# Kernel optimization log

Hardware: AMD Instinct MI355X
Metric: run time of the kernel (lower is better)

Reference implementation:

```python
import jax, jax.numpy as jnp
import numpy as np


def setup_inputs() -> dict:
    key = jax.random.key(0)
    k1, k2, k3 = jax.random.split(key, 3)
    B, N, D = 64, 2048, 1024
    output = jax.random.normal(k1, (B, 1, D), dtype=jnp.float32)
    context = jax.random.normal(k2, (B, N, D), dtype=jnp.float32)
    # nn.Linear(2*dim, dim): weight [dim, 2*dim], bias [dim]
    W_out = jax.random.normal(k3, (D, 2 * D), dtype=jnp.float32) * (1.0 / np.sqrt(2 * D))
    b_out = jnp.zeros((D,), dtype=jnp.float32)
    return {"output": output, "context": context, "W_out": W_out, "b_out": b_out}


def reference(output, context, W_out, b_out):
    B, q, D = output.shape  # q == 1
    N = context.shape[1]
    # scores: (B, q, N) = output @ context^T
    attn = jnp.einsum('bqd,bnd->bqn', output, context)
    attn = jax.nn.softmax(attn, axis=-1)
    # mix: (B, q, D)
    mix = jnp.einsum('bqn,bnd->bqd', attn, context)
    combined = jnp.concatenate([mix, output], axis=-1)  # (B, q, 2D)
    out = jnp.tanh(jnp.einsum('bqe,de->bqd', combined, W_out) + b_out)
    return (out, attn)
```

## Files before the change

### kernel.cpp

```cpp
#include <hip/hip_runtime.h>
#include <cmath>

#define BATCH 64
#define NCTX 2048
#define DIM 1024
#define CHUNKS 16
#define ROWS_PER_CHUNK (NCTX / CHUNKS)
#define ROWS_PER_WAVE (ROWS_PER_CHUNK / 4)

typedef float f4_t __attribute__((ext_vector_type(4)));

__global__ __launch_bounds__(256) void attn_phase1(
    const float* __restrict__ q,
    const float* __restrict__ ctx,
    float* __restrict__ scores,
    float* __restrict__ part_m,
    float* __restrict__ part_l,
    float* __restrict__ part_o)
{
    const int blk  = blockIdx.x;
    const int b    = blk / CHUNKS;
    const int c    = blk % CHUNKS;
    const int tid  = threadIdx.x;
    const int wave = tid >> 6;
    const int lane = tid & 63;

    f4_t qf[4];
    const float* qb = q + (size_t)b * DIM;
    #pragma unroll
    for (int j = 0; j < 4; ++j)
        qf[j] = *reinterpret_cast<const f4_t*>(qb + lane * 4 + 256 * j);

    float m = -INFINITY, l = 0.f;
    f4_t o[4];
    #pragma unroll
    for (int j = 0; j < 4; ++j) o[j] = (f4_t)(0.f);

    const int row0 = c * ROWS_PER_CHUNK + wave * ROWS_PER_WAVE;
    const float* cb = ctx + (size_t)b * NCTX * DIM;
    float* sc = scores + (size_t)b * NCTX;

    for (int i = 0; i < ROWS_PER_WAVE; i += 4) {
        f4_t cf[4][4];
        #pragma unroll
        for (int r = 0; r < 4; ++r) {
            const float* cr = cb + (size_t)(row0 + i + r) * DIM + lane * 4;
            #pragma unroll
            for (int j = 0; j < 4; ++j)
                cf[r][j] = __builtin_nontemporal_load(
                    reinterpret_cast<const f4_t*>(cr + 256 * j));
        }

        float s[4];
        #pragma unroll
        for (int r = 0; r < 4; ++r) {
            float d0 = qf[0].x * cf[r][0].x + qf[0].y * cf[r][0].y
                     + qf[0].z * cf[r][0].z + qf[0].w * cf[r][0].w;
            float d1 = qf[1].x * cf[r][1].x + qf[1].y * cf[r][1].y
                     + qf[1].z * cf[r][1].z + qf[1].w * cf[r][1].w;
            float d2 = qf[2].x * cf[r][2].x + qf[2].y * cf[r][2].y
                     + qf[2].z * cf[r][2].z + qf[2].w * cf[r][2].w;
            float d3 = qf[3].x * cf[r][3].x + qf[3].y * cf[r][3].y
                     + qf[3].z * cf[r][3].z + qf[3].w * cf[r][3].w;
            s[r] = (d0 + d1) + (d2 + d3);
        }

        #pragma unroll
        for (int off = 32; off >= 1; off >>= 1) {
            s[0] += __shfl_xor(s[0], off, 64);
            s[1] += __shfl_xor(s[1], off, 64);
            s[2] += __shfl_xor(s[2], off, 64);
            s[3] += __shfl_xor(s[3], off, 64);
        }

        {
            float sv = (lane == 1) ? s[1] : (lane == 2) ? s[2]
                     : (lane == 3) ? s[3] : s[0];
            if (lane < 4) sc[row0 + i + lane] = sv;
        }

        const float mx = fmaxf(fmaxf(s[0], s[1]), fmaxf(s[2], s[3]));
        const float m_new = fmaxf(m, mx);
        if (m_new > m) {
            const float a = __expf(m - m_new);
            l *= a;
            #pragma unroll
            for (int j = 0; j < 4; ++j) o[j] *= a;
            m = m_new;
        }
        const float p0 = __expf(s[0] - m);
        const float p1 = __expf(s[1] - m);
        const float p2 = __expf(s[2] - m);
        const float p3 = __expf(s[3] - m);
        l += (p0 + p1) + (p2 + p3);
        #pragma unroll
        for (int j = 0; j < 4; ++j) {
            o[j].x += p0 * cf[0][j].x + p1 * cf[1][j].x
                    + p2 * cf[2][j].x + p3 * cf[3][j].x;
            o[j].y += p0 * cf[0][j].y + p1 * cf[1][j].y
                    + p2 * cf[2][j].y + p3 * cf[3][j].y;
            o[j].z += p0 * cf[0][j].z + p1 * cf[1][j].z
                    + p2 * cf[2][j].z + p3 * cf[3][j].z;
            o[j].w += p0 * cf[0][j].w + p1 * cf[1][j].w
                    + p2 * cf[2][j].w + p3 * cf[3][j].w;
        }
    }

    __shared__ float wm[4], wl[4];
    __shared__ float o_lds[4 * DIM];
    if (lane == 0) { wm[wave] = m; wl[wave] = l; }
    __syncthreads();

    const float Mb = fmaxf(fmaxf(wm[0], wm[1]), fmaxf(wm[2], wm[3]));
    float Lb = 0.f;
    #pragma unroll
    for (int w = 0; w < 4; ++w) Lb += wl[w] * __expf(wm[w] - Mb);

    const float aw = __expf(m - Mb);
    #pragma unroll
    for (int j = 0; j < 4; ++j) {
        f4_t t = o[j] * aw;
        *reinterpret_cast<f4_t*>(&o_lds[wave * DIM + lane * 4 + 256 * j]) = t;
    }
    __syncthreads();

    {
        const int e = tid * 4;
        f4_t s0 = *reinterpret_cast<const f4_t*>(&o_lds[0 * DIM + e]);
        f4_t s1 = *reinterpret_cast<const f4_t*>(&o_lds[1 * DIM + e]);
        f4_t s2 = *reinterpret_cast<const f4_t*>(&o_lds[2 * DIM + e]);
        f4_t s3 = *reinterpret_cast<const f4_t*>(&o_lds[3 * DIM + e]);
        f4_t r = (s0 + s1) + (s2 + s3);
        *reinterpret_cast<f4_t*>(&part_o[((size_t)b * CHUNKS + c) * DIM + e]) = r;
    }
    if (tid == 0) {
        part_m[b * CHUNKS + c] = Mb;
        part_l[b * CHUNKS + c] = Lb;
    }
}

__global__ __launch_bounds__(256) void attn_phase2(
    const float* __restrict__ scores,
    const float* __restrict__ part_m,
    const float* __restrict__ part_l,
    const float* __restrict__ part_o,
    float* __restrict__ mix,
    float* __restrict__ attn_out)
{
    const int b    = blockIdx.x >> 2;
    const int part = blockIdx.x & 3;
    const int tid  = threadIdx.x;

    float M = -INFINITY;
    #pragma unroll
    for (int i = 0; i < CHUNKS; ++i) M = fmaxf(M, part_m[b * CHUNKS + i]);

    float w[CHUNKS];
    float L = 0.f;
    #pragma unroll
    for (int i = 0; i < CHUNKS; ++i) {
        w[i] = __expf(part_m[b * CHUNKS + i] - M);
        L += part_l[b * CHUNKS + i] * w[i];
    }
    const float invL = 1.f / L;

    {
        const int e = part * 256 + tid;
        float acc = 0.f;
        #pragma unroll
        for (int i = 0; i < CHUNKS; ++i)
            acc += part_o[((size_t)b * CHUNKS + i) * DIM + e] * w[i];
        mix[(size_t)b * DIM + e] = acc * invL;
    }

    #pragma unroll
    for (int t = 0; t < 2; ++t) {
        const int n = part * 512 + t * 256 + tid;
        attn_out[(size_t)b * NCTX + n] =
            __expf(scores[(size_t)b * NCTX + n] - M) * invL;
    }
}

#define BT 4
#define DT 32
__global__ __launch_bounds__(256) void attn_phase3(
    const float* __restrict__ mix,
    const float* __restrict__ q,
    const float* __restrict__ W,
    const float* __restrict__ bias,
    float* __restrict__ out)
{
    const int d_chunk = blockIdx.x % (DIM / DT);
    const int b_chunk = blockIdx.x / (DIM / DT);
    const int d0 = d_chunk * DT;
    const int b0 = b_chunk * BT;
    const int tid  = threadIdx.x;
    const int wave = tid >> 6;
    const int lane = tid & 63;

    __shared__ float comb[BT * 2 * DIM];
    for (int i = tid; i < BT * 2 * DIM; i += 256) {
        const int bl = i >> 11;
        const int e  = i & 2047;
        comb[i] = (e < DIM) ? mix[(size_t)(b0 + bl) * DIM + e]
                            : q[(size_t)(b0 + bl) * DIM + (e - DIM)];
    }
    __syncthreads();

    const int d_base = d0 + wave * (DT / 4);
    #pragma unroll
    for (int g = 0; g < 2; ++g) {
        const int dg = d_base + g * 4;
        float acc[4][BT];
        #pragma unroll
        for (int di = 0; di < 4; ++di)
            #pragma unroll
            for (int bl = 0; bl < BT; ++bl) acc[di][bl] = 0.f;

        for (int kk = 0; kk < 2 * DIM; kk += 256) {
            f4_t wv[4];
            #pragma unroll
            for (int di = 0; di < 4; ++di)
                wv[di] = *reinterpret_cast<const f4_t*>(
                    W + (size_t)(dg + di) * (2 * DIM) + kk + lane * 4);
            #pragma unroll
            for (int bl = 0; bl < BT; ++bl) {
                f4_t cv = *reinterpret_cast<const f4_t*>(
                    &comb[bl * 2 * DIM + kk + lane * 4]);
                #pragma unroll
                for (int di = 0; di < 4; ++di) {
                    acc[di][bl] += wv[di].x * cv.x;
                    acc[di][bl] += wv[di].y * cv.y;
                    acc[di][bl] += wv[di].z * cv.z;
                    acc[di][bl] += wv[di].w * cv.w;
                }
            }
        }

        float myval = 0.f;
        #pragma unroll
        for (int di = 0; di < 4; ++di) {
            #pragma unroll
            for (int bl = 0; bl < BT; ++bl) {
                float v = acc[di][bl];
                #pragma unroll
                for (int off = 32; off >= 1; off >>= 1)
                    v += __shfl_xor(v, off, 64);
                if (lane == di * BT + bl) myval = v;
            }
        }
        if (lane < 16) {
            const int di = lane >> 2;
            const int bl = lane & 3;
            const int d  = dg + di;
            out[(size_t)(b0 + bl) * DIM + d] = tanhf(myval + bias[d]);
        }
    }
}

extern "C" void kernel_launch(void* const* d_in, const int* in_sizes, int n_in,
                              void* d_out, int out_size, void* d_ws, size_t ws_size,
                              hipStream_t stream) {
    const float* q    = (const float*)d_in[0];
    const float* ctx  = (const float*)d_in[1];
    const float* W    = (const float*)d_in[2];
    const float* bias = (const float*)d_in[3];

    float* out_main = (float*)d_out;
    float* attn_out = (float*)d_out + (size_t)BATCH * DIM;

    float* ws      = (float*)d_ws;
    float* scores  = ws;
    float* part_m  = scores + (size_t)BATCH * NCTX;
    float* part_l  = part_m + BATCH * CHUNKS;
    float* part_o  = part_l + BATCH * CHUNKS;
    float* mix     = part_o + (size_t)BATCH * CHUNKS * DIM;

    attn_phase1<<<BATCH * CHUNKS, 256, 0, stream>>>(q, ctx, scores,
                                                    part_m, part_l, part_o);
    attn_phase2<<<BATCH * 4, 256, 0, stream>>>(scores, part_m, part_l, part_o,
                                               mix, attn_out);
    attn_phase3<<<(DIM / DT) * (BATCH / BT), 256, 0, stream>>>(mix, q, W, bias,
                                                               out_main);
}
```

Before: 675.1 us.

## Double-buffer context row loads in attention phase1 with pairwise processing

Restructures the phase1 loop to process two context rows per iteration while prefetching the next pair into a second register buffer. It also makes the online-softmax rescale branchless and adds a 4-blocks-per-CU launch bound. The intent is to overlap global load latency with compute and raise occupancy. Dynamic indexing of the register buffer and the tighter register cap risk spills, and halving the rows per iteration means fewer loads in flight per wave.

```diff
diff --git a/kernel.cpp b/kernel.cpp
--- a/kernel.cpp
+++ b/kernel.cpp
@@ -7,10 +7,11 @@
 #define CHUNKS 16
 #define ROWS_PER_CHUNK (NCTX / CHUNKS)
 #define ROWS_PER_WAVE (ROWS_PER_CHUNK / 4)
+#define PAIRS (ROWS_PER_WAVE / 2)
 
 typedef float f4_t __attribute__((ext_vector_type(4)));
 
-__global__ __launch_bounds__(256) void attn_phase1(
+__global__ __launch_bounds__(256, 4) void attn_phase1(
     const float* __restrict__ q,
     const float* __restrict__ ctx,
     float* __restrict__ scores,
@@ -40,70 +41,75 @@
     const float* cb = ctx + (size_t)b * NCTX * DIM;
     float* sc = scores + (size_t)b * NCTX;
 
-    for (int i = 0; i < ROWS_PER_WAVE; i += 4) {
-        f4_t cf[4][4];
-        #pragma unroll
-        for (int r = 0; r < 4; ++r) {
-            const float* cr = cb + (size_t)(row0 + i + r) * DIM + lane * 4;
-            #pragma unroll
-            for (int j = 0; j < 4; ++j)
-                cf[r][j] = __builtin_nontemporal_load(
-                    reinterpret_cast<const f4_t*>(cr + 256 * j));
-        }
-
-        float s[4];
-        #pragma unroll
-        for (int r = 0; r < 4; ++r) {
-            float d0 = qf[0].x * cf[r][0].x + qf[0].y * cf[r][0].y
-                     + qf[0].z * cf[r][0].z + qf[0].w * cf[r][0].w;
-            float d1 = qf[1].x * cf[r][1].x + qf[1].y * cf[r][1].y
-                     + qf[1].z * cf[r][1].z + qf[1].w * cf[r][1].w;
-            float d2 = qf[2].x * cf[r][2].x + qf[2].y * cf[r][2].y
-                     + qf[2].z * cf[r][2].z + qf[2].w * cf[r][2].w;
-            float d3 = qf[3].x * cf[r][3].x + qf[3].y * cf[r][3].y
-                     + qf[3].z * cf[r][3].z + qf[3].w * cf[r][3].w;
-            s[r] = (d0 + d1) + (d2 + d3);
+    f4_t cf[2][2][4];
+
+    #pragma unroll
+    for (int r = 0; r < 2; ++r) {
+        const float* cr = cb + (size_t)(row0 + r) * DIM + lane * 4;
+        #pragma unroll
+        for (int j = 0; j < 4; ++j)
+            cf[0][r][j] = __builtin_nontemporal_load(
+                reinterpret_cast<const f4_t*>(cr + 256 * j));
+    }
+
+    for (int p = 0; p < PAIRS; ++p) {
+        const int buf  = p & 1;
+        const int nbuf = buf ^ 1;
+
+        if (p + 1 < PAIRS) {
+            #pragma unroll
+            for (int r = 0; r < 2; ++r) {
+                const float* cr = cb + (size_t)(row0 + (p + 1) * 2 + r) * DIM + lane * 4;
+                #pragma unroll
+                for (int j = 0; j < 4; ++j)
+                    cf[nbuf][r][j] = __builtin_nontemporal_load(
+                        reinterpret_cast<const f4_t*>(cr + 256 * j));
+            }
+        }
+
+        float s0, s1;
+        {
+            float a0 = qf[0].x * cf[buf][0][0].x + qf[0].y * cf[buf][0][0].y
+                     + qf[0].z * cf[buf][0][0].z + qf[0].w * cf[buf][0][0].w;
+            float a1 = qf[1].x * cf[buf][0][1].x + qf[1].y * cf[buf][0][1].y
+                     + qf[1].z * cf[buf][0][1].z + qf[1].w * cf[buf][0][1].w;
+            float a2 = qf[2].x * cf[buf][0][2].x + qf[2].y * cf[buf][0][2].y
+                     + qf[2].z * cf[buf][0][2].z + qf[2].w * cf[buf][0][2].w;
+            float a3 = qf[3].x * cf[buf][0][3].x + qf[3].y * cf[buf][0][3].y
+                     + qf[3].z * cf[buf][0][3].z + qf[3].w * cf[buf][0][3].w;
+            s0 = (a0 + a1) + (a2 + a3);
+            float b0 = qf[0].x * cf[buf][1][0].x + qf[0].y * cf[buf][1][0].y
+                     + qf[0].z * cf[buf][1][0].z + qf[0].w * cf[buf][1][0].w;
+            float b1 = qf[1].x * cf[buf][1][1].x + qf[1].y * cf[buf][1][1].y
+                     + qf[1].z * cf[buf][1][1].z + qf[1].w * cf[buf][1][1].w;
+            float b2 = qf[2].x * cf[buf][1][2].x + qf[2].y * cf[buf][1][2].y
+                     + qf[2].z * cf[buf][1][2].z + qf[2].w * cf[buf][1][2].w;
+            float b3 = qf[3].x * cf[buf][1][3].x + qf[3].y * cf[buf][1][3].y
+                     + qf[3].z * cf[buf][1][3].z + qf[3].w * cf[buf][1][3].w;
+            s1 = (b0 + b1) + (b2 + b3);
         }
 
         #pragma unroll
         for (int off = 32; off >= 1; off >>= 1) {
-            s[0] += __shfl_xor(s[0], off, 64);
-            s[1] += __shfl_xor(s[1], off, 64);
-            s[2] += __shfl_xor(s[2], off, 64);
-            s[3] += __shfl_xor(s[3], off, 64);
-        }
-
-        {
-            float sv = (lane == 1) ? s[1] : (lane == 2) ? s[2]
-                     : (lane == 3) ? s[3] : s[0];
-            if (lane < 4) sc[row0 + i + lane] = sv;
-        }
-
-        const float mx = fmaxf(fmaxf(s[0], s[1]), fmaxf(s[2], s[3]));
-        const float m_new = fmaxf(m, mx);
-        if (m_new > m) {
-            const float a = __expf(m - m_new);
-            l *= a;
-            #pragma unroll
-            for (int j = 0; j < 4; ++j) o[j] *= a;
-            m = m_new;
-        }
-        const float p0 = __expf(s[0] - m);
-        const float p1 = __expf(s[1] - m);
-        const float p2 = __expf(s[2] - m);
-        const float p3 = __expf(s[3] - m);
-        l += (p0 + p1) + (p2 + p3);
+            s0 += __shfl_xor(s0, off, 64);
+            s1 += __shfl_xor(s1, off, 64);
+        }
+
+        const float m_new = fmaxf(m, fmaxf(s0, s1));
+        const float a     = __expf(m - m_new);
+        const float p0    = __expf(s0 - m_new);
+        const float p1    = __expf(s1 - m_new);
+        l = l * a + p0 + p1;
         #pragma unroll
         for (int j = 0; j < 4; ++j) {
-            o[j].x += p0 * cf[0][j].x + p1 * cf[1][j].x
-                    + p2 * cf[2][j].x + p3 * cf[3][j].x;
-            o[j].y += p0 * cf[0][j].y + p1 * cf[1][j].y
-                    + p2 * cf[2][j].y + p3 * cf[3][j].y;
-            o[j].z += p0 * cf[0][j].z + p1 * cf[1][j].z
-                    + p2 * cf[2][j].z + p3 * cf[3][j].z;
-            o[j].w += p0 * cf[0][j].w + p1 * cf[1][j].w
-                    + p2 * cf[2][j].w + p3 * cf[3][j].w;
-        }
+            o[j].x = o[j].x * a + p0 * cf[buf][0][j].x + p1 * cf[buf][1][j].x;
+            o[j].y = o[j].y * a + p0 * cf[buf][0][j].y + p1 * cf[buf][1][j].y;
+            o[j].z = o[j].z * a + p0 * cf[buf][0][j].z + p1 * cf[buf][1][j].z;
+            o[j].w = o[j].w * a + p0 * cf[buf][0][j].w + p1 * cf[buf][1][j].w;
+        }
+        m = m_new;
+
+        if (lane < 2) sc[row0 + p * 2 + lane] = lane ? s1 : s0;
     }
 
     __shared__ float wm[4], wl[4];
```

Measured after the change: 946.9 us. 40.2% more time.
